# Kernel optimization log

Measured on AMD Instinct MI355X. Metric: run time of the kernel, lower is better.

Reference implementation:

```python
import jax, jax.numpy as jnp
import numpy as np

N = 100000
IN_DIM = 256
HID = 128
E = 1600000


def _gcn_conv(x, W, b, src, dst, n_nodes):
    """PyG GCNConv: add self-loops, symmetric normalization, linear transform."""
    xw = x @ W  # [N, H]
    loop = jnp.arange(n_nodes, dtype=src.dtype)
    s = jnp.concatenate([src, loop])  # sources (j)
    d = jnp.concatenate([dst, loop])  # targets (i)
    ones = jnp.ones(s.shape[0], dtype=x.dtype)
    deg = jax.ops.segment_sum(ones, d, num_segments=n_nodes)  # in-degree incl. self-loop
    dinv = jnp.where(deg > 0, jax.lax.rsqrt(deg), 0.0)
    norm = dinv[s] * dinv[d]  # [E+N]
    msgs = xw[s] * norm[:, None]  # gather + scale
    out = jax.ops.segment_sum(msgs, d, num_segments=n_nodes)  # scatter-add at targets
    return out + b


def setup_inputs() -> dict:
    key = jax.random.key(0)
    ks = jax.random.split(key, 12)
    x = jax.random.normal(ks[0], (N, IN_DIM), dtype=jnp.float32)
    edge_index = jax.random.randint(ks[1], (2, E), 0, N, dtype=jnp.int64)
    h_node = jax.random.uniform(ks[2], (N,), dtype=jnp.float32)
    # learned params (glorot-ish scale)
    W1 = jax.random.normal(ks[3], (IN_DIM, HID), dtype=jnp.float32) / np.sqrt(IN_DIM)
    b1 = jnp.zeros((HID,), dtype=jnp.float32)
    W2 = jax.random.normal(ks[4], (HID, HID), dtype=jnp.float32) / np.sqrt(HID)
    b2 = jnp.zeros((HID,), dtype=jnp.float32)
    Wc = jax.random.normal(ks[5], (HID, 2), dtype=jnp.float32) / np.sqrt(HID)
    bc = jnp.zeros((2,), dtype=jnp.float32)
    Wf = jax.random.normal(ks[6], (HID, 2), dtype=jnp.float32) / np.sqrt(HID)
    bf = jnp.zeros((2,), dtype=jnp.float32)
    return {"x": x, "edge_index": edge_index, "h_node": h_node,
            "W1": W1, "b1": b1, "W2": W2, "b2": b2,
            "Wc": Wc, "bc": bc, "Wf": Wf, "bf": bf}


def reference(x, edge_index, h_node, W1, b1, W2, b2, Wc, bc, Wf, bf):
    src, dst = edge_index[0], edge_index[1]
    h1 = jax.nn.relu(_gcn_conv(x, W1, b1, src, dst, x.shape[0]))      # [N, HID]
    logits_coarse = h1 @ Wc + bc                                      # [N, 2]
    alpha = h_node[:, None]                                           # [N, 1]
    h2 = jax.nn.relu(_gcn_conv(h1, W2, b2, src, dst, x.shape[0]))     # [N, HID]
    h2_adaptive = alpha * h2 + (1.0 - alpha) * h1
    logits_fine = h2_adaptive @ Wf + bf                               # [N, 2]
    return 0.5 * logits_coarse + 0.5 * logits_fine
```

## Files before the change

kernel.cpp:

```cpp
#include <hip/hip_runtime.h>


#define HID 128
#define SHIFT 9
#define RANGE 512
#define MAXB 256
#define TILE 4096

typedef __bf16 bf16x8 __attribute__((ext_vector_type(8)));
typedef float  f32x4  __attribute__((ext_vector_type(4)));
typedef float  f32x2  __attribute__((ext_vector_type(2)));

__device__ __forceinline__ unsigned short f2bf(float x) {
    unsigned int b = __float_as_uint(x);
    b += 0x7fffu + ((b >> 16) & 1u);
    return (unsigned short)(b >> 16);
}
__device__ __forceinline__ float bflo(unsigned int u) { return __uint_as_float(u << 16); }
__device__ __forceinline__ float bfhi(unsigned int u) { return __uint_as_float(u & 0xffff0000u); }
__device__ __forceinline__ unsigned packbf(float a, float b) {
    return (unsigned)f2bf(a) | ((unsigned)f2bf(b) << 16);
}

__device__ __forceinline__ void gload_lds16(const void* g, void* l) {
    __builtin_amdgcn_global_load_lds(
        (const __attribute__((address_space(1))) void*)g,
        (__attribute__((address_space(3))) void*)l, 16, 0, 0);
}


__global__ __launch_bounds__(256)
void bincount_kernel(const int* __restrict__ dst, int* __restrict__ bin_counts,
                     int E, int NB) {
    __shared__ int h[MAXB];
    for (int i = threadIdx.x; i < NB; i += 256) h[i] = 0;
    __syncthreads();
    const int base = blockIdx.x * TILE;
#pragma unroll
    for (int j = 0; j < TILE; j += 256) {
        int e = base + j + threadIdx.x;
        if (e < E) atomicAdd(&h[((unsigned)dst[e]) >> SHIFT], 1);
    }
    __syncthreads();
    for (int i = threadIdx.x; i < NB; i += 256) {
        int v = h[i];
        if (v) atomicAdd(&bin_counts[i], v);
    }
}

__global__ void binscan_kernel(const int* __restrict__ bin_counts,
                               int* __restrict__ bin_off, int* __restrict__ bin_cur, int NB) {
    __shared__ int sh[MAXB];
    const int t = threadIdx.x;
    int v = (t < NB) ? bin_counts[t] : 0;
    sh[t] = v;
    __syncthreads();
    for (int s = 1; s < 256; s <<= 1) {
        int x = (t >= s) ? sh[t - s] : 0;
        __syncthreads();
        sh[t] += x;
        __syncthreads();
    }
    if (t < NB) {
        int ex = sh[t] - v;
        bin_off[t] = ex;
        bin_cur[t] = ex;
    }
}

__global__ __launch_bounds__(256)
void stage_kernel(const int* __restrict__ src, const int* __restrict__ dst,
                  int* __restrict__ bin_cur, unsigned* __restrict__ pairs, int E) {
    __shared__ int sh_hist[MAXB];
    __shared__ int sh_off[MAXB];
    __shared__ int sh_ex[MAXB];
    __shared__ int sh_gbase[MAXB];
    __shared__ uint2 stg[TILE];
    const int t = threadIdx.x;
    const int base = blockIdx.x * TILE;
    const int cnt = min(TILE, E - base);

    for (int i = t; i < MAXB; i += 256) sh_hist[i] = 0;
    __syncthreads();

    int s[16], d[16], r[16];
#pragma unroll
    for (int j = 0; j < 16; ++j) {
        const int k = j * 256 + t;
        if (k < cnt) {
            s[j] = src[base + k];
            d[j] = dst[base + k];
            r[j] = atomicAdd(&sh_hist[((unsigned)d[j]) >> SHIFT], 1);
        }
    }
    __syncthreads();

    const int hv = sh_hist[t];
    sh_off[t] = hv;
    __syncthreads();
    for (int st = 1; st < 256; st <<= 1) {
        int x = (t >= st) ? sh_off[t - st] : 0;
        __syncthreads();
        sh_off[t] += x;
        __syncthreads();
    }
    sh_ex[t] = sh_off[t] - hv;
    if (hv > 0) sh_gbase[t] = atomicAdd(&bin_cur[t], hv);
    __syncthreads();

#pragma unroll
    for (int j = 0; j < 16; ++j) {
        const int k = j * 256 + t;
        if (k < cnt) {
            int b = ((unsigned)d[j]) >> SHIFT;
            stg[sh_ex[b] + r[j]] = make_uint2((unsigned)s[j], (unsigned)d[j]);
        }
    }
    __syncthreads();

    for (int i = t; i < cnt; i += 256) {
        uint2 p = stg[i];
        int b = (int)(p.y >> SHIFT);
        unsigned w = ((p.y & (RANGE - 1)) << 23) | p.x;
        pairs[sh_gbase[b] + (i - sh_ex[b])] = w;
    }
}

__global__ __launch_bounds__(256)
void binrowp_kernel(const unsigned* __restrict__ pairs, const int* __restrict__ bin_off,
                    float* __restrict__ dinv, int* __restrict__ rowp,
                    int N, int NB, int E) {
    __shared__ int c[RANGE];
    __shared__ int sh[256];
    const int b = blockIdx.x;
    const int t = threadIdx.x;
    const int nb = b << SHIFT;
    const int nr = min(RANGE, N - nb);
    for (int i = t; i < RANGE; i += 256) c[i] = 0;
    __syncthreads();
    const int lo = bin_off[b];
    const int hi = (b + 1 < NB) ? bin_off[b + 1] : E;
    for (int i = lo + t; i < hi; i += 256)
        atomicAdd(&c[pairs[i] >> 23], 1);
    __syncthreads();
    const int v0 = c[2 * t], v1 = c[2 * t + 1];
    const int pr = v0 + v1;
    sh[t] = pr;
    __syncthreads();
    for (int s = 1; s < 256; s <<= 1) {
        int x = (t >= s) ? sh[t - s] : 0;
        __syncthreads();
        sh[t] += x;
        __syncthreads();
    }
    const int ex = sh[t] - pr + lo;
    if (2 * t < nr) {
        rowp[nb + 2 * t] = ex;
        dinv[nb + 2 * t] = rsqrtf((float)(v0 + 1));
    }
    if (2 * t + 1 < nr) {
        rowp[nb + 2 * t + 1] = ex + v0;
        dinv[nb + 2 * t + 1] = rsqrtf((float)(v1 + 1));
    }
    if (b == 0 && t == 0) rowp[N] = E;
}

__global__ __launch_bounds__(256)
void fine_kernel(const unsigned* __restrict__ pairs, const int* __restrict__ bin_off,
                 const int* __restrict__ rowp, const float* __restrict__ dinv,
                 unsigned* __restrict__ colv1, int N, int NB, int E) {
    __shared__ int cur[RANGE];
    const int b = blockIdx.x;
    const int nb = b << SHIFT;
    const int nr = min(RANGE, N - nb);
    for (int i = threadIdx.x; i < nr; i += 256) cur[i] = rowp[nb + i];
    __syncthreads();
    const int lo = bin_off[b];
    const int hi = (b + 1 < NB) ? bin_off[b + 1] : E;
    for (int i = lo + threadIdx.x; i < hi; i += 256) {
        unsigned w = pairs[i];
        unsigned s = w & 0x7fffffu;
        int pos = atomicAdd(&cur[w >> 23], 1);
        unsigned w15 = __float2uint_rn(dinv[s] * 32767.0f);
        colv1[pos] = (s << 15) | w15;
    }
}

__global__ void prep_kernel(const float* __restrict__ W1, const float* __restrict__ W2,
                            unsigned short* __restrict__ wt1, unsigned short* __restrict__ wt2,
                            int K1, int* __restrict__ bin_counts) {
    int idx = blockIdx.x * 256 + threadIdx.x;
    if (idx < MAXB) bin_counts[idx] = 0;
    if (idx < 128 * K1) {
        int nn = idx / K1, k = idx - nn * K1;
        wt1[(size_t)nn * K1 + k] = f2bf(W1[(size_t)k * 128 + nn]);
    }
    if (idx < 128 * 128) {
        int nn = idx >> 7, k = idx & 127;
        wt2[(size_t)nn * 128 + k] = f2bf(W2[(size_t)k * 128 + nn]);
    }
}

template <bool A_BF16>
__global__ __launch_bounds__(256)
void gemm_kernel(const void* __restrict__ Aptr, const unsigned short* __restrict__ Wt,
                 unsigned short* __restrict__ Out, int nrows, int K) {
    __shared__ __align__(16) char tilebuf[16384];
    const int tid  = threadIdx.x;
    const int wave = tid >> 6;
    const int lane = tid & 63;
    const int q = lane >> 4;
    const int r = lane & 15;
    const int blkrow = blockIdx.x * 128;
    const int wrow = blkrow + wave * 32;

    f32x4 acc[2][8];
#pragma unroll
    for (int s = 0; s < 2; ++s)
#pragma unroll
        for (int c = 0; c < 8; ++c) acc[s][c] = (f32x4){0.f, 0.f, 0.f, 0.f};

    for (int k0 = 0; k0 < K; k0 += 32) {
        if (A_BF16) {
            const unsigned short* A = (const unsigned short*)Aptr;
#pragma unroll
            for (int c = 0; c < 2; ++c) {
                const int u = tid + c * 256;
                const int l = u & 63;
                const int g = u >> 6;
                int row = blkrow + (g >> 1) * 32 + (g & 1) * 16 + (l & 15);
                row = min(row, nrows - 1);
                const int k = k0 + (l >> 4) * 8;
                gload_lds16(A + (size_t)row * K + k,
                            tilebuf + c * 4096 + wave * 1024);
            }
        } else {
            const float* A = (const float*)Aptr;
#pragma unroll
            for (int c = 0; c < 4; ++c) {
                const int u = tid + c * 256;
                const int l = u & 63;
                const int g = u >> 6;
                const int half = g & 1;
                const int ws = g >> 1;
                int row = blkrow + (ws >> 1) * 32 + (ws & 1) * 16 + (l & 15);
                row = min(row, nrows - 1);
                const int k = k0 + (l >> 4) * 8 + half * 4;
                gload_lds16(A + (size_t)row * K + k,
                            tilebuf + c * 4096 + wave * 1024);
            }
        }
        __syncthreads();

        const int kk = k0 + q * 8;
        bf16x8 afrag[2];
#pragma unroll
        for (int s = 0; s < 2; ++s) {
            if (A_BF16) {
                afrag[s] = *reinterpret_cast<const bf16x8*>(
                    tilebuf + ((wave * 2 + s) * 64 + lane) * 16);
            } else {
                const float4 x0 = *reinterpret_cast<const float4*>(
                    tilebuf + (((wave * 2 + s) * 2 + 0) * 64 + lane) * 16);
                const float4 x1 = *reinterpret_cast<const float4*>(
                    tilebuf + (((wave * 2 + s) * 2 + 1) * 64 + lane) * 16);
                bf16x8 a;
                a[0] = (__bf16)x0.x; a[1] = (__bf16)x0.y; a[2] = (__bf16)x0.z; a[3] = (__bf16)x0.w;
                a[4] = (__bf16)x1.x; a[5] = (__bf16)x1.y; a[6] = (__bf16)x1.z; a[7] = (__bf16)x1.w;
                afrag[s] = a;
            }
        }
#pragma unroll
        for (int c = 0; c < 8; ++c) {
            const bf16x8 b = *reinterpret_cast<const bf16x8*>(Wt + (size_t)(c * 16 + r) * K + kk);
#pragma unroll
            for (int s = 0; s < 2; ++s)
                acc[s][c] = __builtin_amdgcn_mfma_f32_16x16x32_bf16(afrag[s], b, acc[s][c], 0, 0, 0);
        }
        __syncthreads();
    }
#pragma unroll
    for (int s = 0; s < 2; ++s)
#pragma unroll
        for (int v = 0; v < 4; ++v) {
            const int row = wrow + s * 16 + q * 4 + v;
            if (row < nrows) {
#pragma unroll
                for (int c = 0; c < 8; ++c)
                    Out[(size_t)row * 128 + c * 16 + r] = f2bf(acc[s][c][v]);
            }
        }
}


#define AGG_EDGE_LOOP(XW)                                                      \
    for (int base = beg; base < end; base += 64) {                             \
        const int e = base + lane;                                             \
        const unsigned cw = (e < end) ? colv1[e] : 0u;                         \
        const int cnt = min(64, end - base);                                   \
        _Pragma("unroll 4")                                                    \
        for (int t = 0; t < cnt; t += 4) {                                     \
            const unsigned cg = (unsigned)__shfl((int)cw, t + q4);             \
            const unsigned st = cg >> 15;                                      \
            const float    wt = (float)(cg & 0x7fffu) * (1.0f / 32767.0f);     \
            const uint4 uu = *reinterpret_cast<const uint4*>(                  \
                (const char*)(XW) + ((st << 8) + coff));                       \
            A0 += (f32x2){bflo(uu.x), bfhi(uu.x)} * wt;                        \
            A1 += (f32x2){bflo(uu.y), bfhi(uu.y)} * wt;                        \
            A2 += (f32x2){bflo(uu.z), bfhi(uu.z)} * wt;                        \
            A3 += (f32x2){bflo(uu.w), bfhi(uu.w)} * wt;                        \
        }                                                                      \
    }                                                                          \
    A0 += __shfl_xor(A0, 16); A1 += __shfl_xor(A1, 16);                        \
    A2 += __shfl_xor(A2, 16); A3 += __shfl_xor(A3, 16);                        \
    A0 += __shfl_xor(A0, 32); A1 += __shfl_xor(A1, 32);                        \
    A2 += __shfl_xor(A2, 32); A3 += __shfl_xor(A3, 32);

__device__ __forceinline__ f32x2 __shfl_xor(f32x2 v, int m) {
    return (f32x2){__shfl_xor(v[0], m), __shfl_xor(v[1], m)};
}

__global__ __launch_bounds__(256)
void agg1_kernel(const unsigned short* __restrict__ xw, const unsigned* __restrict__ colv1,
                 const int* __restrict__ rowp, const float* __restrict__ dinv,
                 const float* __restrict__ b1, const float* __restrict__ Wc,
                 const float* __restrict__ bc, uint4* __restrict__ h1,
                 float* __restrict__ outp, int n) {
    const int node = blockIdx.x * 4 + (threadIdx.x >> 6);
    if (node >= n) return;
    const int lane = threadIdx.x & 63;
    const int c    = lane & 15;
    const int q4   = lane >> 4;
    const unsigned coff = (unsigned)c << 4;
    const float di = dinv[node];

    f32x2 A0 = {0.f,0.f}, A1 = {0.f,0.f}, A2 = {0.f,0.f}, A3 = {0.f,0.f};
    {
        const float ws = (q4 == 0) ? di : 0.f;
        const uint4 uu = *reinterpret_cast<const uint4*>(
            (const char*)xw + (((unsigned)node << 8) + coff));
        A0 += (f32x2){bflo(uu.x), bfhi(uu.x)} * ws;
        A1 += (f32x2){bflo(uu.y), bfhi(uu.y)} * ws;
        A2 += (f32x2){bflo(uu.z), bfhi(uu.z)} * ws;
        A3 += (f32x2){bflo(uu.w), bfhi(uu.w)} * ws;
    }

    const int beg = rowp[node], end = rowp[node + 1];
    AGG_EDGE_LOOP(xw)

    const float4 bb0 = reinterpret_cast<const float4*>(b1)[2*c];
    const float4 bb1 = reinterpret_cast<const float4*>(b1)[2*c + 1];
    float a0 = fmaxf(A0[0]*di + bb0.x, 0.f), a1 = fmaxf(A0[1]*di + bb0.y, 0.f);
    float a2 = fmaxf(A1[0]*di + bb0.z, 0.f), a3 = fmaxf(A1[1]*di + bb0.w, 0.f);
    float a4 = fmaxf(A2[0]*di + bb1.x, 0.f), a5 = fmaxf(A2[1]*di + bb1.y, 0.f);
    float a6 = fmaxf(A3[0]*di + bb1.z, 0.f), a7 = fmaxf(A3[1]*di + bb1.w, 0.f);

    if (q4 == 0)
        h1[((unsigned)node << 4) + c] =
            make_uint4(packbf(a0,a1), packbf(a2,a3), packbf(a4,a5), packbf(a6,a7));

    const float4 w0 = reinterpret_cast<const float4*>(Wc)[4*c];
    const float4 w1 = reinterpret_cast<const float4*>(Wc)[4*c + 1];
    const float4 w2 = reinterpret_cast<const float4*>(Wc)[4*c + 2];
    const float4 w3 = reinterpret_cast<const float4*>(Wc)[4*c + 3];
    float c0 = a0*w0.x + a1*w0.z + a2*w1.x + a3*w1.z
             + a4*w2.x + a5*w2.z + a6*w3.x + a7*w3.z;
    float c1 = a0*w0.y + a1*w0.w + a2*w1.y + a3*w1.w
             + a4*w2.y + a5*w2.w + a6*w3.y + a7*w3.w;
    if (q4) { c0 = 0.f; c1 = 0.f; }
#pragma unroll
    for (int off = 32; off; off >>= 1) {
        c0 += __shfl_down(c0, off);
        c1 += __shfl_down(c1, off);
    }
    if (lane == 0) {
        outp[2 * (size_t)node]     = 0.5f * (c0 + bc[0]);
        outp[2 * (size_t)node + 1] = 0.5f * (c1 + bc[1]);
    }
}

__global__ __launch_bounds__(256)
void agg2_kernel(const unsigned short* __restrict__ xw2, const uint4* __restrict__ h1,
                 const unsigned* __restrict__ colv1, const int* __restrict__ rowp,
                 const float* __restrict__ dinv, const float* __restrict__ b2,
                 const float* __restrict__ Wf, const float* __restrict__ bfv,
                 const float* __restrict__ hnode, float* __restrict__ outp, int n) {
    const int node = blockIdx.x * 4 + (threadIdx.x >> 6);
    if (node >= n) return;
    const int lane = threadIdx.x & 63;
    const int c    = lane & 15;
    const int q4   = lane >> 4;
    const unsigned coff = (unsigned)c << 4;
    const float di = dinv[node];

    f32x2 A0 = {0.f,0.f}, A1 = {0.f,0.f}, A2 = {0.f,0.f}, A3 = {0.f,0.f};
    {
        const float ws = (q4 == 0) ? di : 0.f;
        const uint4 uu = *reinterpret_cast<const uint4*>(
            (const char*)xw2 + (((unsigned)node << 8) + coff));
        A0 += (f32x2){bflo(uu.x), bfhi(uu.x)} * ws;
        A1 += (f32x2){bflo(uu.y), bfhi(uu.y)} * ws;
        A2 += (f32x2){bflo(uu.z), bfhi(uu.z)} * ws;
        A3 += (f32x2){bflo(uu.w), bfhi(uu.w)} * ws;
    }

    const int beg = rowp[node], end = rowp[node + 1];
    AGG_EDGE_LOOP(xw2)

    const float4 bb0 = reinterpret_cast<const float4*>(b2)[2*c];
    const float4 bb1 = reinterpret_cast<const float4*>(b2)[2*c + 1];
    float h20 = fmaxf(A0[0]*di + bb0.x, 0.f), h21 = fmaxf(A0[1]*di + bb0.y, 0.f);
    float h22 = fmaxf(A1[0]*di + bb0.z, 0.f), h23 = fmaxf(A1[1]*di + bb0.w, 0.f);
    float h24 = fmaxf(A2[0]*di + bb1.x, 0.f), h25 = fmaxf(A2[1]*di + bb1.y, 0.f);
    float h26 = fmaxf(A3[0]*di + bb1.z, 0.f), h27 = fmaxf(A3[1]*di + bb1.w, 0.f);

    const float alpha = hnode[node];
    const float beta  = 1.f - alpha;
    const uint4 hh = h1[((unsigned)node << 4) + c];
    const float ha0 = alpha*h20 + beta*bflo(hh.x);
    const float ha1 = alpha*h21 + beta*bfhi(hh.x);
    const float ha2 = alpha*h22 + beta*bflo(hh.y);
    const float ha3 = alpha*h23 + beta*bfhi(hh.y);
    const float ha4 = alpha*h24 + beta*bflo(hh.z);
    const float ha5 = alpha*h25 + beta*bfhi(hh.z);
    const float ha6 = alpha*h26 + beta*bflo(hh.w);
    const float ha7 = alpha*h27 + beta*bfhi(hh.w);

    const float4 w0 = reinterpret_cast<const float4*>(Wf)[4*c];
    const float4 w1 = reinterpret_cast<const float4*>(Wf)[4*c + 1];
    const float4 w2 = reinterpret_cast<const float4*>(Wf)[4*c + 2];
    const float4 w3 = reinterpret_cast<const float4*>(Wf)[4*c + 3];
    float f0 = ha0*w0.x + ha1*w0.z + ha2*w1.x + ha3*w1.z
             + ha4*w2.x + ha5*w2.z + ha6*w3.x + ha7*w3.z;
    float f1 = ha0*w0.y + ha1*w0.w + ha2*w1.y + ha3*w1.w
             + ha4*w2.y + ha5*w2.w + ha6*w3.y + ha7*w3.w;
    if (q4) { f0 = 0.f; f1 = 0.f; }
#pragma unroll
    for (int off = 32; off; off >>= 1) {
        f0 += __shfl_down(f0, off);
        f1 += __shfl_down(f1, off);
    }
    if (lane == 0) {
        outp[2 * (size_t)node]     += 0.5f * (f0 + bfv[0]);
        outp[2 * (size_t)node + 1] += 0.5f * (f1 + bfv[1]);
    }
}


extern "C" void kernel_launch(void* const* d_in, const int* in_sizes, int n_in,
                              void* d_out, int out_size, void* d_ws, size_t ws_size,
                              hipStream_t stream) {
    const float* x     = (const float*)d_in[0];
    const int*   ei    = (const int*)d_in[1];
    const float* hnode = (const float*)d_in[2];
    const float* W1    = (const float*)d_in[3];
    const float* b1    = (const float*)d_in[4];
    const float* W2    = (const float*)d_in[5];
    const float* b2    = (const float*)d_in[6];
    const float* Wc    = (const float*)d_in[7];
    const float* bc    = (const float*)d_in[8];
    const float* Wf    = (const float*)d_in[9];
    const float* bfv   = (const float*)d_in[10];

    const int N  = in_sizes[2];
    const int E  = in_sizes[1] / 2;
    const int K1 = in_sizes[3] / HID;
    const int NB = (N + RANGE - 1) >> SHIFT;
    const int* srcv = ei;
    const int* dstv = ei + E;
    float* outp = (float*)d_out;

    char* ws = (char*)d_ws;
    size_t off = 0;
    auto alloc = [&](size_t bytes) -> char* {
        char* p = ws + off;
        off += (bytes + 255) & ~(size_t)255;
        return p;
    };
    unsigned short* xw       = (unsigned short*)alloc((size_t)N * HID * 2);
    unsigned short* h1       = (unsigned short*)alloc((size_t)N * HID * 2);
    float*          dinv     = (float*)alloc((size_t)N * 4);
    int*            rowp     = (int*)alloc((size_t)(N + 1) * 4);
    unsigned*       colv1    = (unsigned*)alloc((size_t)E * 4);
    unsigned*       pairs    = (unsigned*)alloc((size_t)E * 4);
    int*            bin_counts = (int*)alloc(MAXB * 4);
    int*            bin_off    = (int*)alloc(MAXB * 4);
    int*            bin_cur    = (int*)alloc(MAXB * 4);
    unsigned short* wt1      = (unsigned short*)alloc((size_t)HID * K1 * 2);
    unsigned short* wt2      = (unsigned short*)alloc((size_t)HID * HID * 2);

    prep_kernel<<<(HID * K1 + 255) / 256, 256, 0, stream>>>(W1, W2, wt1, wt2, K1, bin_counts);

    const int ntiles = (E + TILE - 1) / TILE;
    bincount_kernel<<<ntiles, 256, 0, stream>>>(dstv, bin_counts, E, NB);
    binscan_kernel<<<1, 256, 0, stream>>>(bin_counts, bin_off, bin_cur, NB);
    stage_kernel<<<ntiles, 256, 0, stream>>>(srcv, dstv, bin_cur, pairs, E);
    binrowp_kernel<<<NB, 256, 0, stream>>>(pairs, bin_off, dinv, rowp, N, NB, E);
    fine_kernel<<<NB, 256, 0, stream>>>(pairs, bin_off, rowp, dinv, colv1, N, NB, E);

    gemm_kernel<false><<<(N + 127) / 128, 256, 0, stream>>>((const void*)x, wt1, xw, N, K1);
    agg1_kernel<<<(N + 3) / 4, 256, 0, stream>>>(xw, colv1, rowp, dinv,
                                                 b1, Wc, bc, (uint4*)h1, outp, N);
    gemm_kernel<true><<<(N + 127) / 128, 256, 0, stream>>>((const void*)h1, wt2, xw, N, HID);
    agg2_kernel<<<(N + 3) / 4, 256, 0, stream>>>(xw, (const uint4*)h1, colv1,
                                                 rowp, dinv, b2, Wf, bfv, hnode, outp, N);
}
```

Measured before the change: 445.7 us.

## Replace LDS-staged GEMM with register-prefetched direct loads and compile-time K

The GEMM kernel no longer stages A tiles through LDS with global_load_lds and block-wide barriers. Each lane now loads its own A fragments straight into registers, with a software prefetch ring up to four K-steps deep, and K becomes a template parameter so the loop fully unrolls. The aim is to remove barrier stalls and hide global load latency behind the MFMA work. In exchange, register pressure rises (the fp32 path holds 16 float4 prefetch buffers plus 8 B fragments), which may lower occupancy, and the per-lane global accesses may coalesce less well.

```diff
diff --git a/kernel.cpp b/kernel.cpp
--- a/kernel.cpp
+++ b/kernel.cpp
@@ -20,12 +20,6 @@
 __device__ __forceinline__ float bfhi(unsigned int u) { return __uint_as_float(u & 0xffff0000u); }
 __device__ __forceinline__ unsigned packbf(float a, float b) {
     return (unsigned)f2bf(a) | ((unsigned)f2bf(b) << 16);
-}
-
-__device__ __forceinline__ void gload_lds16(const void* g, void* l) {
-    __builtin_amdgcn_global_load_lds(
-        (const __attribute__((address_space(1))) void*)g,
-        (__attribute__((address_space(3))) void*)l, 16, 0, 0);
 }
 
 
@@ -201,18 +195,23 @@
     }
 }
 
-template <bool A_BF16>
+template <bool A_BF16, int K>
 __global__ __launch_bounds__(256)
 void gemm_kernel(const void* __restrict__ Aptr, const unsigned short* __restrict__ Wt,
-                 unsigned short* __restrict__ Out, int nrows, int K) {
-    __shared__ __align__(16) char tilebuf[16384];
+                 unsigned short* __restrict__ Out, int nrows) {
+    constexpr int NIT = K / 32;
+    constexpr int DEPTH = (NIT < 4) ? NIT : 4;
     const int tid  = threadIdx.x;
     const int wave = tid >> 6;
     const int lane = tid & 63;
     const int q = lane >> 4;
     const int r = lane & 15;
-    const int blkrow = blockIdx.x * 128;
-    const int wrow = blkrow + wave * 32;
+    const int wrow = blockIdx.x * 128 + wave * 32;
+    const size_t row0 = (size_t)min(wrow + r,      nrows - 1);
+    const size_t row1 = (size_t)min(wrow + 16 + r, nrows - 1);
+
+    const unsigned short* A16 = (const unsigned short*)Aptr;
+    const float*          A32 = (const float*)Aptr;
 
     f32x4 acc[2][8];
 #pragma unroll
@@ -220,65 +219,68 @@
 #pragma unroll
         for (int c = 0; c < 8; ++c) acc[s][c] = (f32x4){0.f, 0.f, 0.f, 0.f};
 
-    for (int k0 = 0; k0 < K; k0 += 32) {
+    bf16x8 preb[DEPTH][2];
+    float4 pref[DEPTH][2][2];
+
+#pragma unroll
+    for (int i = 0; i < DEPTH; ++i) {
+        const int kk = i * 32 + q * 8;
         if (A_BF16) {
-            const unsigned short* A = (const unsigned short*)Aptr;
-#pragma unroll
-            for (int c = 0; c < 2; ++c) {
-                const int u = tid + c * 256;
-                const int l = u & 63;
-                const int g = u >> 6;
-                int row = blkrow + (g >> 1) * 32 + (g & 1) * 16 + (l & 15);
-                row = min(row, nrows - 1);
-                const int k = k0 + (l >> 4) * 8;
-                gload_lds16(A + (size_t)row * K + k,
-                            tilebuf + c * 4096 + wave * 1024);
-            }
+            preb[i][0] = *reinterpret_cast<const bf16x8*>(A16 + row0 * K + kk);
+            preb[i][1] = *reinterpret_cast<const bf16x8*>(A16 + row1 * K + kk);
         } else {
-            const float* A = (const float*)Aptr;
-#pragma unroll
-            for (int c = 0; c < 4; ++c) {
-                const int u = tid + c * 256;
-                const int l = u & 63;
-                const int g = u >> 6;
-                const int half = g & 1;
-                const int ws = g >> 1;
-                int row = blkrow + (ws >> 1) * 32 + (ws & 1) * 16 + (l & 15);
-                row = min(row, nrows - 1);
-                const int k = k0 + (l >> 4) * 8 + half * 4;
-                gload_lds16(A + (size_t)row * K + k,
-                            tilebuf + c * 4096 + wave * 1024);
-            }
-        }
-        __syncthreads();
-
-        const int kk = k0 + q * 8;
+            pref[i][0][0] = *reinterpret_cast<const float4*>(A32 + row0 * K + kk);
+            pref[i][0][1] = *reinterpret_cast<const float4*>(A32 + row0 * K + kk + 4);
+            pref[i][1][0] = *reinterpret_cast<const float4*>(A32 + row1 * K + kk);
+            pref[i][1][1] = *reinterpret_cast<const float4*>(A32 + row1 * K + kk + 4);
+        }
+    }
+
+#pragma unroll
+    for (int it = 0; it < NIT; ++it) {
+        const int slot = it % DEPTH;
+        const int kk = it * 32 + q * 8;
+
+        bf16x8 bfr[8];
+#pragma unroll
+        for (int c = 0; c < 8; ++c)
+            bfr[c] = *reinterpret_cast<const bf16x8*>(Wt + (size_t)(c * 16 + r) * K + kk);
+
         bf16x8 afrag[2];
 #pragma unroll
         for (int s = 0; s < 2; ++s) {
             if (A_BF16) {
-                afrag[s] = *reinterpret_cast<const bf16x8*>(
-                    tilebuf + ((wave * 2 + s) * 64 + lane) * 16);
+                afrag[s] = preb[slot][s];
             } else {
-                const float4 x0 = *reinterpret_cast<const float4*>(
-                    tilebuf + (((wave * 2 + s) * 2 + 0) * 64 + lane) * 16);
-                const float4 x1 = *reinterpret_cast<const float4*>(
-                    tilebuf + (((wave * 2 + s) * 2 + 1) * 64 + lane) * 16);
+                const float4 x0 = pref[slot][s][0];
+                const float4 x1 = pref[slot][s][1];
                 bf16x8 a;
                 a[0] = (__bf16)x0.x; a[1] = (__bf16)x0.y; a[2] = (__bf16)x0.z; a[3] = (__bf16)x0.w;
                 a[4] = (__bf16)x1.x; a[5] = (__bf16)x1.y; a[6] = (__bf16)x1.z; a[7] = (__bf16)x1.w;
                 afrag[s] = a;
             }
         }
+
+        if (it + DEPTH < NIT) {
+            const int kk2 = (it + DEPTH) * 32 + q * 8;
+            if (A_BF16) {
+                preb[slot][0] = *reinterpret_cast<const bf16x8*>(A16 + row0 * K + kk2);
+                preb[slot][1] = *reinterpret_cast<const bf16x8*>(A16 + row1 * K + kk2);
+            } else {
+                pref[slot][0][0] = *reinterpret_cast<const float4*>(A32 + row0 * K + kk2);
+                pref[slot][0][1] = *reinterpret_cast<const float4*>(A32 + row0 * K + kk2 + 4);
+                pref[slot][1][0] = *reinterpret_cast<const float4*>(A32 + row1 * K + kk2);
+                pref[slot][1][1] = *reinterpret_cast<const float4*>(A32 + row1 * K + kk2 + 4);
+            }
+        }
+
 #pragma unroll
         for (int c = 0; c < 8; ++c) {
-            const bf16x8 b = *reinterpret_cast<const bf16x8*>(Wt + (size_t)(c * 16 + r) * K + kk);
-#pragma unroll
-            for (int s = 0; s < 2; ++s)
-                acc[s][c] = __builtin_amdgcn_mfma_f32_16x16x32_bf16(afrag[s], b, acc[s][c], 0, 0, 0);
-        }
-        __syncthreads();
-    }
+            acc[0][c] = __builtin_amdgcn_mfma_f32_16x16x32_bf16(afrag[0], bfr[c], acc[0][c], 0, 0, 0);
+            acc[1][c] = __builtin_amdgcn_mfma_f32_16x16x32_bf16(afrag[1], bfr[c], acc[1][c], 0, 0, 0);
+        }
+    }
+
 #pragma unroll
     for (int s = 0; s < 2; ++s)
 #pragma unroll
@@ -498,10 +500,10 @@
     binrowp_kernel<<<NB, 256, 0, stream>>>(pairs, bin_off, dinv, rowp, N, NB, E);
     fine_kernel<<<NB, 256, 0, stream>>>(pairs, bin_off, rowp, dinv, colv1, N, NB, E);
 
-    gemm_kernel<false><<<(N + 127) / 128, 256, 0, stream>>>((const void*)x, wt1, xw, N, K1);
+    gemm_kernel<false, 256><<<(N + 127) / 128, 256, 0, stream>>>((const void*)x, wt1, xw, N);
     agg1_kernel<<<(N + 3) / 4, 256, 0, stream>>>(xw, colv1, rowp, dinv,
                                                  b1, Wc, bc, (uint4*)h1, outp, N);
-    gemm_kernel<true><<<(N + 127) / 128, 256, 0, stream>>>((const void*)h1, wt2, xw, N, HID);
+    gemm_kernel<true, 128><<<(N + 127) / 128, 256, 0, stream>>>((const void*)h1, wt2, xw, N);
     agg2_kernel<<<(N + 3) / 4, 256, 0, stream>>>(xw, (const uint4*)h1, colv1,
                                                  rowp, dinv, b2, Wf, bfv, hnode, outp, N);
 }
```

Result: faster. 432.8 us (-2.9%).
